# Optimization experiments

Measured on AMD Instinct MI355X. Metric: run time of the kernel, lower is better.

## Reference

```python
import jax, jax.numpy as jnp
import numpy as np

H, C = 8, 32          # heads, channels per head; H*C = 256 triggers the LN branch
N_NODES = 30000       # nodes per node type
N_EDGES = 100000      # edges per edge type
N_TYPES = 6           # hardwired edge types (all src = Package_Name)
D_IN = 128            # raw input feature dim (Package_Name stays at 128)
LRELU_SLOPE = 0.2     # PyG GATConv default negative_slope


def _segment_softmax(e, dst, n):
    # softmax of per-edge logits e [E,H] grouped by destination node
    m = jax.ops.segment_max(e, dst, num_segments=n)
    ex = jnp.exp(e - m[dst])
    den = jax.ops.segment_sum(ex, dst, num_segments=n)
    return ex / (den[dst] + 1e-16)


def _gat(x_src, x_tgt, src, dst, Ws, Wd, a_s, a_d, b):
    # bipartite GATConv, concat heads, no self loops, no edge features
    hs = (x_src @ Ws).reshape(-1, H, C)   # [Ns,H,C]
    hd = (x_tgt @ Wd).reshape(-1, H, C)   # [Nt,H,C]
    es = jnp.einsum('nhc,hc->nh', hs, a_s)
    ed = jnp.einsum('nhc,hc->nh', hd, a_d)
    e = jax.nn.leaky_relu(es[src] + ed[dst], negative_slope=LRELU_SLOPE)  # [E,H]
    n = x_tgt.shape[0]
    alpha = _segment_softmax(e, dst, n)                                   # [E,H]
    msg = hs[src] * alpha[:, :, None]                                     # [E,H,C]
    out = jax.ops.segment_sum(msg, dst, num_segments=n).reshape(n, H * C) + b
    return out, alpha


def _ln_relu(x, g, b):
    mu = x.mean(-1, keepdims=True)
    var = ((x - mu) ** 2).mean(-1, keepdims=True)
    return jax.nn.relu((x - mu) / jnp.sqrt(var + 1e-5) * g + b)


def setup_inputs() -> dict:
    key = jax.random.key(0)
    ks = jax.random.split(key, 16)
    s = 0.05
    return {
        'x_pkg': jax.random.normal(ks[0], (N_NODES, D_IN), jnp.float32),
        'x_tgt': jax.random.normal(ks[1], (N_TYPES, N_NODES, D_IN), jnp.float32),
        'edge_index': jax.random.randint(ks[2], (N_TYPES, 2, N_EDGES), 0, N_NODES, jnp.int32),
        'W1_src': jax.random.normal(ks[3], (N_TYPES, D_IN, H * C), jnp.float32) * s,
        'W1_dst': jax.random.normal(ks[4], (N_TYPES, D_IN, H * C), jnp.float32) * s,
        'att1_src': jax.random.normal(ks[5], (N_TYPES, H, C), jnp.float32) * s,
        'att1_dst': jax.random.normal(ks[6], (N_TYPES, H, C), jnp.float32) * s,
        'b1': jnp.zeros((N_TYPES, H * C), jnp.float32),
        'W2_src': jax.random.normal(ks[7], (N_TYPES, D_IN, H * C), jnp.float32) * s,
        'W2_dst': jax.random.normal(ks[8], (N_TYPES, H * C, H * C), jnp.float32) * s,
        'att2_src': jax.random.normal(ks[9], (N_TYPES, H, C), jnp.float32) * s,
        'att2_dst': jax.random.normal(ks[10], (N_TYPES, H, C), jnp.float32) * s,
        'b2': jnp.zeros((N_TYPES, H * C), jnp.float32),
        'gamma': jnp.ones((N_TYPES, H * C), jnp.float32),
        'beta': jnp.zeros((N_TYPES, H * C), jnp.float32),
        'Wc': jax.random.normal(ks[11], (N_TYPES * H * C + D_IN, 1), jnp.float32) * s,
        'bc': jnp.zeros((1,), jnp.float32),
    }


def reference(x_pkg, x_tgt, edge_index, W1_src, W1_dst, att1_src, att1_dst, b1,
              W2_src, W2_dst, att2_src, att2_dst, b2, gamma, beta, Wc, bc):
    def layer(xt, ei, Ws, Wd, a_s, a_d, bb):
        return _gat(x_pkg, xt, ei[0], ei[1], Ws, Wd, a_s, a_d, bb)

    vlayer = jax.vmap(layer, in_axes=(0, 0, 0, 0, 0, 0, 0))

    # layer 1: Package_Name -> each of 6 target types; Package_Name itself unchanged
    out1, _ = vlayer(x_tgt, edge_index, W1_src, W1_dst, att1_src, att1_dst, b1)
    x1 = jax.vmap(_ln_relu)(out1, gamma, beta)   # module reuses ln1 after both layers

    # layer 2: src features are still the raw 128-d Package_Name features
    out2, alpha2 = vlayer(x1, edge_index, W2_src, W2_dst, att2_src, att2_dst, b2)
    x2 = jax.vmap(_ln_relu)(out2, gamma, beta)

    # global mean pool per node type, concat (6 targets then Package_Name), classify
    pooled = jnp.concatenate([x2.mean(axis=1).reshape(-1), x_pkg.mean(axis=0)])
    logits = pooled @ Wc[:, 0] + bc[0]
    return logits, alpha2
```

## Files before the change

kernel.cpp:

```cpp
#include <hip/hip_runtime.h>
#include <hip/hip_bf16.h>
#include <cstddef>

#define N_NODES 30000
#define N_EDGES 100000
#define N_TYPES 6
#define D_IN 128
#define HC 256
#define NH 8
#define CH 32

typedef __attribute__((ext_vector_type(8))) unsigned short ushort8_t;
typedef __attribute__((ext_vector_type(4))) unsigned short ushort4_t;
typedef __attribute__((ext_vector_type(8))) __bf16 bf16x8;
typedef __attribute__((ext_vector_type(4))) float floatx4;

#define FG_GRID (N_NODES / 4)

__device__ inline unsigned short f2bf(float f) {
    unsigned u = __float_as_uint(f);
    u += 0x7fffu + ((u >> 16) & 1u);
    return (unsigned short)(u >> 16);
}
__device__ inline float bf2f(unsigned short u) {
    return __uint_as_float(((unsigned)u) << 16);
}

__global__ void zero4(float4* __restrict__ p, int n4) {
    int g = blockIdx.x * blockDim.x + threadIdx.x;
    if (g < n4) p[g] = make_float4(0.f, 0.f, 0.f, 0.f);
}
__global__ void zero_i(int* __restrict__ p, int n) {
    int g = blockIdx.x * blockDim.x + threadIdx.x;
    if (g < n) p[g] = 0;
}
__global__ void to_bf16(const float* __restrict__ x, unsigned short* __restrict__ o, int n4) {
    int g = blockIdx.x * blockDim.x + threadIdx.x;
    if (g >= n4) return;
    float4 v = ((const float4*)x)[g];
    ushort4_t p;
    p[0] = f2bf(v.x); p[1] = f2bf(v.y); p[2] = f2bf(v.z); p[3] = f2bf(v.w);
    *(ushort4_t*)&o[(size_t)g * 4] = p;
}

__global__ void hist_all(const int* __restrict__ ei, int* __restrict__ counts) {
    int t = blockIdx.y;
    int e = blockIdx.x * 256 + threadIdx.x;
    if (e < N_EDGES)
        atomicAdd(&counts[t * N_NODES + ei[(size_t)t * 2 * N_EDGES + N_EDGES + e]], 1);
}

#define SCAN_T 1024
#define SCAN_C 30
__global__ __launch_bounds__(1024) void scan_all(const int* __restrict__ counts_g,
                                                 int* __restrict__ row_ptr_g,
                                                 int* __restrict__ cursor_g) {
    int t = blockIdx.x;
    const int* counts = counts_g + t * N_NODES;
    int* row_ptr = row_ptr_g + t * (N_NODES + 1);
    int* cursor = cursor_g + t * N_NODES;
    __shared__ int part[SCAN_T];
    int tid = threadIdx.x;
    int base = tid * SCAN_C;
    int loc[SCAN_C];
    int s = 0;
    #pragma unroll
    for (int i = 0; i < SCAN_C; ++i) {
        int idx = base + i;
        int v = (idx < N_NODES) ? counts[idx] : 0;
        loc[i] = s; s += v;
    }
    part[tid] = s;
    __syncthreads();
    int tot = s;
    for (int d = 1; d < SCAN_T; d <<= 1) {
        int v = (tid >= d) ? part[tid - d] : 0;
        __syncthreads();
        part[tid] += v;
        __syncthreads();
    }
    int off = part[tid] - tot;
    #pragma unroll
    for (int i = 0; i < SCAN_C; ++i) {
        int idx = base + i;
        if (idx < N_NODES) { int r = off + loc[i]; row_ptr[idx] = r; cursor[idx] = r; }
    }
    if (tid == SCAN_T - 1) row_ptr[N_NODES] = part[SCAN_T - 1];
}

__global__ void fill_all(const int* __restrict__ ei, int* __restrict__ cursor,
                         int* __restrict__ elist) {
    int t = blockIdx.y;
    int e = blockIdx.x * 256 + threadIdx.x;
    if (e < N_EDGES) {
        const int* src = ei + (size_t)t * 2 * N_EDGES;
        const int* dst = src + N_EDGES;
        int pos = atomicAdd(&cursor[t * N_NODES + dst[e]], 1);
        elist[t * N_EDGES + pos] = src[e];
    }
}

__global__ void att_weight_all(const float* __restrict__ W1d, const float* __restrict__ a1d,
                               const float* __restrict__ W2d, const float* __restrict__ a2d,
                               float* __restrict__ wd1, float* __restrict__ wd2) {
    int g = blockIdx.x * blockDim.x + threadIdx.x;
    const int per_t = (D_IN + HC) * NH;
    if (g >= N_TYPES * per_t) return;
    int t = g / per_t, r = g % per_t;
    if (r < D_IN * NH) {
        int k = r >> 3, h = r & 7;
        const float* wr = W1d + (size_t)t * D_IN * HC + (size_t)k * HC + h * CH;
        const float* ar = a1d + t * HC + h * CH;
        float s = 0.f;
        #pragma unroll
        for (int c = 0; c < CH; ++c) s += wr[c] * ar[c];
        wd1[t * D_IN * NH + h * D_IN + k] = s;
    } else {
        r -= D_IN * NH;
        int k = r >> 3, h = r & 7;
        const float* wr = W2d + (size_t)t * HC * HC + (size_t)k * HC + h * CH;
        const float* ar = a2d + t * HC + h * CH;
        float s = 0.f;
        #pragma unroll
        for (int c = 0; c < CH; ++c) s += wr[c] * ar[c];
        wd2[t * HC * NH + h * HC + k] = s;
    }
}

__global__ __launch_bounds__(256) void wt_prep(const float* __restrict__ W1s,
                                               const float* __restrict__ W2s,
                                               unsigned short* __restrict__ Wt) {
    const int j = blockIdx.z;
    const float* W = (j < 6) ? W1s + (size_t)j * D_IN * HC
                             : W2s + (size_t)(j - 6) * D_IN * HC;
    const int n0 = blockIdx.x * 64;
    const int k0 = blockIdx.y * 32;
    __shared__ unsigned short tile[32][71];
    const int t = threadIdx.x;
    {
        const int k = t >> 3, n = (t & 7) * 8;
        const float4 a = *(const float4*)&W[(size_t)(k0 + k) * HC + n0 + n];
        const float4 b = *(const float4*)&W[(size_t)(k0 + k) * HC + n0 + n + 4];
        tile[k][n + 0] = f2bf(a.x); tile[k][n + 1] = f2bf(a.y);
        tile[k][n + 2] = f2bf(a.z); tile[k][n + 3] = f2bf(a.w);
        tile[k][n + 4] = f2bf(b.x); tile[k][n + 5] = f2bf(b.y);
        tile[k][n + 6] = f2bf(b.z); tile[k][n + 7] = f2bf(b.w);
    }
    __syncthreads();
    {
        const int n = t >> 2, k = (t & 3) * 8;
        ushort8_t v;
        #pragma unroll
        for (int q = 0; q < 8; ++q) v[q] = tile[k + q][n];
        *(ushort8_t*)&Wt[((size_t)j * HC + n0 + n) * D_IN + k0 + k] = v;
    }
}

__global__ __launch_bounds__(256) void ed1_all(const float* __restrict__ x_tgt,
                                               const float* __restrict__ wd1,
                                               float* __restrict__ ed1g) {
    const int t = blockIdx.y;
    const int lane = threadIdx.x & 63;
    const int wv = threadIdx.x >> 6;
    const int n8 = lane >> 3, h = lane & 7;
    const int node = blockIdx.x * 32 + wv * 8 + n8;
    if (node >= N_NODES) return;
    const float* xr = x_tgt + ((size_t)t * N_NODES + node) * D_IN;
    const float* wp = wd1 + t * D_IN * NH + h * D_IN;
    float acc = 0.f;
    #pragma unroll
    for (int k = 0; k < D_IN; k += 4) {
        const float4 x4 = *(const float4*)&xr[k];
        const float4 w4 = *(const float4*)&wp[k];
        acc += x4.x * w4.x + x4.y * w4.y + x4.z * w4.z + x4.w * w4.w;
    }
    ed1g[((size_t)t * N_NODES + node) * NH + h] = acc;
}

__global__ __launch_bounds__(256) void gemm_all(const unsigned short* __restrict__ A,
                                                const unsigned short* __restrict__ Wt,
                                                const float* __restrict__ att1,
                                                const float* __restrict__ att2,
                                                unsigned short* __restrict__ hs_all,
                                                float* __restrict__ es_all) {
    const int j = blockIdx.z;
    const unsigned short* B = Wt + (size_t)j * HC * D_IN;
    const float* att = (j < 6) ? att1 + j * HC : att2 + (j - 6) * HC;
    unsigned short* Cp = hs_all + (size_t)j * N_NODES * HC;
    float* e_out = es_all + (size_t)j * N_NODES * NH;

    __shared__ __align__(16) unsigned short As[64 * 136];

    const int tid = threadIdx.x;
    const int w = tid >> 6;
    const int lane = tid & 63;
    const int col = lane & 15;
    const int quad = lane >> 4;
    const int m0 = blockIdx.x * 64;
    const int n0 = blockIdx.y * 64;

    {
        const int r = tid >> 2;
        const int kc = (tid & 3) * 8;
        const int gm = m0 + r;
        #pragma unroll
        for (int c = 0; c < 4; ++c) {
            ushort8_t v = (ushort8_t){0, 0, 0, 0, 0, 0, 0, 0};
            if (gm < N_NODES) v = *(const ushort8_t*)&A[(size_t)gm * D_IN + kc + c * 32];
            *(ushort8_t*)&As[r * 136 + kc + c * 32] = v;
        }
    }
    __syncthreads();

    floatx4 acc[4];
    #pragma unroll
    for (int ct = 0; ct < 4; ++ct) acc[ct] = (floatx4){0.f, 0.f, 0.f, 0.f};

    #pragma unroll
    for (int ks = 0; ks < 4; ++ks) {
        ushort8_t araw = *(const ushort8_t*)&As[(w * 16 + col) * 136 + quad * 8 + ks * 32];
        bf16x8 af = __builtin_bit_cast(bf16x8, araw);
        #pragma unroll
        for (int ct = 0; ct < 4; ++ct) {
            ushort8_t braw = *(const ushort8_t*)&B[(size_t)(n0 + ct * 16 + col) * D_IN + quad * 8 + ks * 32];
            bf16x8 bf = __builtin_bit_cast(bf16x8, braw);
            acc[ct] = __builtin_amdgcn_mfma_f32_16x16x32_bf16(af, bf, acc[ct], 0, 0, 0);
        }
    }

    #pragma unroll
    for (int ct = 0; ct < 4; ++ct) {
        #pragma unroll
        for (int r = 0; r < 4; ++r) {
            int gm = m0 + w * 16 + quad * 4 + r;
            if (gm < N_NODES) Cp[(size_t)gm * HC + n0 + ct * 16 + col] = f2bf(acc[ct][r]);
        }
    }

    float attv[4];
    #pragma unroll
    for (int ct = 0; ct < 4; ++ct) attv[ct] = att[n0 + ct * 16 + col];
    const int hbase = n0 >> 5;
    #pragma unroll
    for (int r = 0; r < 4; ++r) {
        float h0v = acc[0][r] * attv[0] + acc[1][r] * attv[1];
        float h1v = acc[2][r] * attv[2] + acc[3][r] * attv[3];
        #pragma unroll
        for (int off = 1; off < 16; off <<= 1) {
            h0v += __shfl_xor(h0v, off);
            h1v += __shfl_xor(h1v, off);
        }
        if (col == 0) {
            int gm = m0 + w * 16 + quad * 4 + r;
            if (gm < N_NODES) {
                e_out[gm * NH + hbase] = h0v;
                e_out[gm * NH + hbase + 1] = h1v;
            }
        }
    }
}

__device__ inline void edge4(const float* __restrict__ es,
                             const unsigned short* __restrict__ hs,
                             int s_pre, int i, int cm,
                             int h_l, int lane, float ed_mine,
                             float& den, float4& acc) {
    const int i1 = (i + 1 < cm) ? i + 1 : cm;
    const int i2 = (i + 2 < cm) ? i + 2 : cm;
    const int i3 = (i + 3 < cm) ? i + 3 : cm;
    const int s0 = __shfl(s_pre, i);
    const int s1 = __shfl(s_pre, i1);
    const int s2 = __shfl(s_pre, i2);
    const int s3 = __shfl(s_pre, i3);
    float q0 = es[s0 * NH + h_l];
    float q1 = es[s1 * NH + h_l];
    float q2 = es[s2 * NH + h_l];
    float q3 = es[s3 * NH + h_l];
    const ushort4_t v0 = *(const ushort4_t*)&hs[(size_t)s0 * HC + lane * 4];
    const ushort4_t v1 = *(const ushort4_t*)&hs[(size_t)s1 * HC + lane * 4];
    const ushort4_t v2 = *(const ushort4_t*)&hs[(size_t)s2 * HC + lane * 4];
    const ushort4_t v3 = *(const ushort4_t*)&hs[(size_t)s3 * HC + lane * 4];
    q0 += ed_mine; q0 = (q0 >= 0.f) ? q0 : 0.2f * q0;
    q1 += ed_mine; q1 = (q1 >= 0.f) ? q1 : 0.2f * q1;
    q2 += ed_mine; q2 = (q2 >= 0.f) ? q2 : 0.2f * q2;
    q3 += ed_mine; q3 = (q3 >= 0.f) ? q3 : 0.2f * q3;
    const float x0 = __expf(q0);
    const float x1 = (i + 1 <= cm) ? __expf(q1) : 0.f;
    const float x2 = (i + 2 <= cm) ? __expf(q2) : 0.f;
    const float x3 = (i + 3 <= cm) ? __expf(q3) : 0.f;
    den += (x0 + x1) + (x2 + x3);
    acc.x += x0 * bf2f(v0[0]) + x1 * bf2f(v1[0]) + x2 * bf2f(v2[0]) + x3 * bf2f(v3[0]);
    acc.y += x0 * bf2f(v0[1]) + x1 * bf2f(v1[1]) + x2 * bf2f(v2[1]) + x3 * bf2f(v3[1]);
    acc.z += x0 * bf2f(v0[2]) + x1 * bf2f(v1[2]) + x2 * bf2f(v2[2]) + x3 * bf2f(v3[2]);
    acc.w += x0 * bf2f(v0[3]) + x1 * bf2f(v1[3]) + x2 * bf2f(v2[3]) + x3 * bf2f(v3[3]);
}

__device__ inline void edge1(const float* __restrict__ es,
                             const unsigned short* __restrict__ hs,
                             int s, int h_l, int lane, float ed_mine,
                             float& den, float4& acc) {
    float x = es[s * NH + h_l] + ed_mine;
    x = (x >= 0.f) ? x : 0.2f * x;
    const float ex = __expf(x);
    den += ex;
    const ushort4_t hv = *(const ushort4_t*)&hs[(size_t)s * HC + lane * 4];
    acc.x += ex * bf2f(hv[0]); acc.y += ex * bf2f(hv[1]);
    acc.z += ex * bf2f(hv[2]); acc.w += ex * bf2f(hv[3]);
}

__global__ __launch_bounds__(256) void fused_gather_all(
        const int* __restrict__ row_ptr_g, const int* __restrict__ elist_g,
        const float* __restrict__ es_all, const float* __restrict__ ed1g,
        const unsigned short* __restrict__ hs_all,
        const float* __restrict__ b1, const float* __restrict__ b2,
        const float* __restrict__ gamma, const float* __restrict__ beta,
        const float* __restrict__ wd2,
        float* __restrict__ ed2g_all, float* __restrict__ deng_all,
        float* __restrict__ ppart) {
    const int t = blockIdx.y;
    const int* row_ptr = row_ptr_g + t * (N_NODES + 1);
    const int* elist = elist_g + t * N_EDGES;
    const float* es1 = es_all + (size_t)t * N_NODES * NH;
    const float* es2 = es_all + (size_t)(6 + t) * N_NODES * NH;
    const unsigned short* hs1 = hs_all + (size_t)t * N_NODES * HC;
    const unsigned short* hs2 = hs_all + (size_t)(6 + t) * N_NODES * HC;
    const float* gam = gamma + t * HC;
    const float* bet = beta + t * HC;
    const float* w2 = wd2 + t * HC * NH;
    float* ed2g = ed2g_all + (size_t)t * N_NODES * NH;
    float* deng = deng_all + (size_t)t * N_NODES * NH;

    const int lane = threadIdx.x & 63;
    const int w = threadIdx.x >> 6;
    const int d = blockIdx.x * 4 + w;
    const int h_l = lane >> 3;

    const float ed_mine = ed1g[((size_t)t * N_NODES + d) * NH + h_l];
    const int e0 = row_ptr[d], e1n = row_ptr[d + 1];
    const int cnt = e1n - e0;
    int s_pre = 0;
    if (lane < cnt) s_pre = elist[e0 + lane];

    float den1 = 0.f, den2 = 0.f;
    float4 acc1 = make_float4(0.f, 0.f, 0.f, 0.f);
    float4 acc2 = make_float4(0.f, 0.f, 0.f, 0.f);

    float q20, q21, q22, q23;
    ushort4_t v20, v21, v22, v23;
    const bool fast = (cnt > 0) && (cnt <= 4);

    if (fast) {
        const int cm = cnt - 1;
        const int s0 = __shfl(s_pre, 0);
        const int s1 = __shfl(s_pre, (1 < cm) ? 1 : cm);
        const int s2 = __shfl(s_pre, (2 < cm) ? 2 : cm);
        const int s3 = __shfl(s_pre, cm);
        float q10 = es1[s0 * NH + h_l];
        float q11 = es1[s1 * NH + h_l];
        float q12 = es1[s2 * NH + h_l];
        float q13 = es1[s3 * NH + h_l];
        const ushort4_t v10 = *(const ushort4_t*)&hs1[(size_t)s0 * HC + lane * 4];
        const ushort4_t v11 = *(const ushort4_t*)&hs1[(size_t)s1 * HC + lane * 4];
        const ushort4_t v12 = *(const ushort4_t*)&hs1[(size_t)s2 * HC + lane * 4];
        const ushort4_t v13 = *(const ushort4_t*)&hs1[(size_t)s3 * HC + lane * 4];
        q20 = es2[s0 * NH + h_l];
        q21 = es2[s1 * NH + h_l];
        q22 = es2[s2 * NH + h_l];
        q23 = es2[s3 * NH + h_l];
        v20 = *(const ushort4_t*)&hs2[(size_t)s0 * HC + lane * 4];
        v21 = *(const ushort4_t*)&hs2[(size_t)s1 * HC + lane * 4];
        v22 = *(const ushort4_t*)&hs2[(size_t)s2 * HC + lane * 4];
        v23 = *(const ushort4_t*)&hs2[(size_t)s3 * HC + lane * 4];
        q10 += ed_mine; q10 = (q10 >= 0.f) ? q10 : 0.2f * q10;
        q11 += ed_mine; q11 = (q11 >= 0.f) ? q11 : 0.2f * q11;
        q12 += ed_mine; q12 = (q12 >= 0.f) ? q12 : 0.2f * q12;
        q13 += ed_mine; q13 = (q13 >= 0.f) ? q13 : 0.2f * q13;
        const float x0 = __expf(q10);
        const float x1 = (cnt > 1) ? __expf(q11) : 0.f;
        const float x2 = (cnt > 2) ? __expf(q12) : 0.f;
        const float x3 = (cnt > 3) ? __expf(q13) : 0.f;
        den1 = (x0 + x1) + (x2 + x3);
        acc1.x = x0 * bf2f(v10[0]) + x1 * bf2f(v11[0]) + x2 * bf2f(v12[0]) + x3 * bf2f(v13[0]);
        acc1.y = x0 * bf2f(v10[1]) + x1 * bf2f(v11[1]) + x2 * bf2f(v12[1]) + x3 * bf2f(v13[1]);
        acc1.z = x0 * bf2f(v10[2]) + x1 * bf2f(v11[2]) + x2 * bf2f(v12[2]) + x3 * bf2f(v13[2]);
        acc1.w = x0 * bf2f(v10[3]) + x1 * bf2f(v11[3]) + x2 * bf2f(v12[3]) + x3 * bf2f(v13[3]);
    } else if (cnt > 0) {
        const int c1 = (cnt < 64) ? cnt : 64;
        const int cm = c1 - 1;
        for (int i = 0; i < c1; i += 4)
            edge4(es1, hs1, s_pre, i, cm, h_l, lane, ed_mine, den1, acc1);
        if (cnt > 64)
            for (int ii = e0 + 64; ii < e1n; ++ii)
                edge1(es1, hs1, elist[ii], h_l, lane, ed_mine, den1, acc1);
    }

    const float inv1 = 1.f / (den1 + 1e-16f);
    const float4 bv1 = *(const float4*)&b1[t * HC + lane * 4];
    acc1.x = acc1.x * inv1 + bv1.x; acc1.y = acc1.y * inv1 + bv1.y;
    acc1.z = acc1.z * inv1 + bv1.z; acc1.w = acc1.w * inv1 + bv1.w;

    float s1 = acc1.x + acc1.y + acc1.z + acc1.w;
    float s2 = acc1.x * acc1.x + acc1.y * acc1.y + acc1.z * acc1.z + acc1.w * acc1.w;
    #pragma unroll
    for (int off = 1; off < 64; off <<= 1) { s1 += __shfl_xor(s1, off); s2 += __shfl_xor(s2, off); }
    const float mu = s1 * (1.f / 256.f);
    const float var = s2 * (1.f / 256.f) - mu * mu;
    const float rstd = rsqrtf(var + 1e-5f);
    const float4 g4 = *(const float4*)&gam[lane * 4];
    const float4 b4 = *(const float4*)&bet[lane * 4];
    const float ya0 = fmaxf((acc1.x - mu) * rstd * g4.x + b4.x, 0.f);
    const float ya1 = fmaxf((acc1.y - mu) * rstd * g4.y + b4.y, 0.f);
    const float ya2 = fmaxf((acc1.z - mu) * rstd * g4.z + b4.z, 0.f);
    const float ya3 = fmaxf((acc1.w - mu) * rstd * g4.w + b4.w, 0.f);

    __shared__ __align__(16) float ya_s[4][256];
    {
        const int c0 = lane * 4;
        const int widx = (c0 & ~31) | ((c0 & 31) ^ ((lane >> 3) << 2));
        *(float4*)&ya_s[w][widx] = make_float4(ya0, ya1, ya2, ya3);
    }
    const int k8 = lane >> 3;
    const int hh = lane & 7;
    const float* w2h = w2 + hh * HC;
    float e2 = 0.f;
    #pragma unroll
    for (int jj = 0; jj < 8; ++jj) {
        const int idx = k8 * 32 + ((jj * 4) ^ (k8 << 2));
        const float4 y = *(const float4*)&ya_s[w][idx];
        const float4 wv = *(const float4*)&w2h[k8 * 32 + jj * 4];
        e2 += y.x * wv.x + y.y * wv.y + y.z * wv.z + y.w * wv.w;
    }
    e2 += __shfl_xor(e2, 8);
    e2 += __shfl_xor(e2, 16);
    e2 += __shfl_xor(e2, 32);
    if (lane < 8) ed2g[d * NH + lane] = e2;
    const float ed2_mine = __shfl(e2, h_l);

    if (fast) {
        q20 += ed2_mine; q20 = (q20 >= 0.f) ? q20 : 0.2f * q20;
        q21 += ed2_mine; q21 = (q21 >= 0.f) ? q21 : 0.2f * q21;
        q22 += ed2_mine; q22 = (q22 >= 0.f) ? q22 : 0.2f * q22;
        q23 += ed2_mine; q23 = (q23 >= 0.f) ? q23 : 0.2f * q23;
        const float x0 = __expf(q20);
        const float x1 = (cnt > 1) ? __expf(q21) : 0.f;
        const float x2 = (cnt > 2) ? __expf(q22) : 0.f;
        const float x3 = (cnt > 3) ? __expf(q23) : 0.f;
        den2 = (x0 + x1) + (x2 + x3);
        acc2.x = x0 * bf2f(v20[0]) + x1 * bf2f(v21[0]) + x2 * bf2f(v22[0]) + x3 * bf2f(v23[0]);
        acc2.y = x0 * bf2f(v20[1]) + x1 * bf2f(v21[1]) + x2 * bf2f(v22[1]) + x3 * bf2f(v23[1]);
        acc2.z = x0 * bf2f(v20[2]) + x1 * bf2f(v21[2]) + x2 * bf2f(v22[2]) + x3 * bf2f(v23[2]);
        acc2.w = x0 * bf2f(v20[3]) + x1 * bf2f(v21[3]) + x2 * bf2f(v22[3]) + x3 * bf2f(v23[3]);
    } else if (cnt > 0) {
        const int c1 = (cnt < 64) ? cnt : 64;
        const int cm = c1 - 1;
        for (int i = 0; i < c1; i += 4)
            edge4(es2, hs2, s_pre, i, cm, h_l, lane, ed2_mine, den2, acc2);
        if (cnt > 64)
            for (int ii = e0 + 64; ii < e1n; ++ii)
                edge1(es2, hs2, elist[ii], h_l, lane, ed2_mine, den2, acc2);
    }

    if ((lane & 7) == 0) deng[d * NH + h_l] = den2;
    const float inv2 = 1.f / (den2 + 1e-16f);
    const float4 bv2 = *(const float4*)&b2[t * HC + lane * 4];
    acc2.x = acc2.x * inv2 + bv2.x; acc2.y = acc2.y * inv2 + bv2.y;
    acc2.z = acc2.z * inv2 + bv2.z; acc2.w = acc2.w * inv2 + bv2.w;

    float t1 = acc2.x + acc2.y + acc2.z + acc2.w;
    float t2 = acc2.x * acc2.x + acc2.y * acc2.y + acc2.z * acc2.z + acc2.w * acc2.w;
    #pragma unroll
    for (int off = 1; off < 64; off <<= 1) { t1 += __shfl_xor(t1, off); t2 += __shfl_xor(t2, off); }
    const float mu2 = t1 * (1.f / 256.f);
    const float var2 = t2 * (1.f / 256.f) - mu2 * mu2;
    const float rstd2 = rsqrtf(var2 + 1e-5f);
    float4 pool;
    pool.x = fmaxf((acc2.x - mu2) * rstd2 * g4.x + b4.x, 0.f);
    pool.y = fmaxf((acc2.y - mu2) * rstd2 * g4.y + b4.y, 0.f);
    pool.z = fmaxf((acc2.z - mu2) * rstd2 * g4.z + b4.z, 0.f);
    pool.w = fmaxf((acc2.w - mu2) * rstd2 * g4.w + b4.w, 0.f);

    __shared__ __align__(16) float sacc[4][260];
    *(float4*)&sacc[w][lane * 4] = pool;
    __syncthreads();
    const int tid = threadIdx.x;
    float tot = sacc[0][tid] + sacc[1][tid] + sacc[2][tid] + sacc[3][tid];
    ppart[((size_t)t * FG_GRID + blockIdx.x) * HC + tid] = tot;
}

__global__ __launch_bounds__(256) void pool_reduce_all(const float* __restrict__ ppart,
                                                       float* __restrict__ psums) {
    int t = blockIdx.y;
    const float* part = ppart + (size_t)t * FG_GRID * HC;
    int tid = threadIdx.x;
    float acc = 0.f;
    for (int b = blockIdx.x; b < FG_GRID; b += gridDim.x)
        acc += part[(size_t)b * HC + tid];
    atomicAdd(&psums[t * HC + tid], acc);
}

__global__ __launch_bounds__(256) void alpha_all(const int* __restrict__ ei,
                          const float* __restrict__ es_all,
                          const float* __restrict__ ed2g_all,
                          const float* __restrict__ deng_all,
                          float* __restrict__ out) {
    int t = blockIdx.y;
    int e = blockIdx.x * 256 + threadIdx.x;
    if (e >= N_EDGES) return;
    const int* src = ei + (size_t)t * 2 * N_EDGES;
    const int* dst = src + N_EDGES;
    const int s = src[e], d = dst[e];
    const float* esp = es_all + (size_t)(6 + t) * N_NODES * NH + (size_t)s * NH;
    const float* edp = ed2g_all + (size_t)t * N_NODES * NH + (size_t)d * NH;
    const float* dnp = deng_all + (size_t)t * N_NODES * NH + (size_t)d * NH;
    const float4 ea = *(const float4*)esp;
    const float4 eb = *(const float4*)(esp + 4);
    const float4 da = *(const float4*)edp;
    const float4 db = *(const float4*)(edp + 4);
    const float4 na = *(const float4*)dnp;
    const float4 nb = *(const float4*)(dnp + 4);
    float x[8];
    x[0] = ea.x + da.x; x[1] = ea.y + da.y; x[2] = ea.z + da.z; x[3] = ea.w + da.w;
    x[4] = eb.x + db.x; x[5] = eb.y + db.y; x[6] = eb.z + db.z; x[7] = eb.w + db.w;
    float n[8] = {na.x, na.y, na.z, na.w, nb.x, nb.y, nb.z, nb.w};
    float* op = out + (size_t)t * N_EDGES * NH + (size_t)e * NH;
    #pragma unroll
    for (int h = 0; h < 8; ++h) {
        float v = x[h];
        v = (v >= 0.f) ? v : 0.2f * v;
        op[h] = __expf(v) / (n[h] + 1e-16f);
    }
}

__global__ __launch_bounds__(256) void pkg_accum(const float* __restrict__ x, float* __restrict__ sums) {
    int tid = threadIdx.x;
    int col = tid & 127;
    int rof = tid >> 7;
    float acc = 0.f;
    for (int r = blockIdx.x * 2 + rof; r < N_NODES; r += gridDim.x * 2)
        acc += x[(size_t)r * D_IN + col];
    atomicAdd(&sums[col], acc);
}

__global__ __launch_bounds__(256) void logits_k(const float* __restrict__ psums,
                                                const float* __restrict__ ksums,
                                                const float* __restrict__ Wc,
                                                const float* __restrict__ bc,
                                                float* __restrict__ out) {
    int tid = threadIdx.x;
    const float inv = 1.f / (float)N_NODES;
    float acc = 0.f;
    for (int i = tid; i < N_TYPES * HC; i += 256) acc += psums[i] * inv * Wc[i];
    if (tid < D_IN) acc += ksums[tid] * inv * Wc[N_TYPES * HC + tid];
    #pragma unroll
    for (int off = 32; off; off >>= 1) acc += __shfl_down(acc, off);
    __shared__ float w[4];
    if ((tid & 63) == 0) w[tid >> 6] = acc;
    __syncthreads();
    if (tid == 0) out[0] = w[0] + w[1] + w[2] + w[3] + bc[0];
}

static inline void zf(float* p, int n, hipStream_t stream) {
    int n4 = (n + 3) >> 2;
    zero4<<<(n4 + 255) / 256, 256, 0, stream>>>((float4*)p, n4);
}

extern "C" void kernel_launch(void* const* d_in, const int* in_sizes, int n_in,
                              void* d_out, int out_size, void* d_ws, size_t ws_size,
                              hipStream_t stream) {
    const float* x_pkg    = (const float*)d_in[0];
    const float* x_tgt    = (const float*)d_in[1];
    const int*   ei       = (const int*)d_in[2];
    const float* W1_src   = (const float*)d_in[3];
    const float* W1_dst   = (const float*)d_in[4];
    const float* att1_src = (const float*)d_in[5];
    const float* att1_dst = (const float*)d_in[6];
    const float* b1       = (const float*)d_in[7];
    const float* W2_src   = (const float*)d_in[8];
    const float* W2_dst   = (const float*)d_in[9];
    const float* att2_src = (const float*)d_in[10];
    const float* att2_dst = (const float*)d_in[11];
    const float* b2       = (const float*)d_in[12];
    const float* gamma    = (const float*)d_in[13];
    const float* beta     = (const float*)d_in[14];
    const float* Wc       = (const float*)d_in[15];
    const float* bc       = (const float*)d_in[16];
    float* out = (float*)d_out;

    char* wsb = (char*)d_ws;
    unsigned short* xpkg_bf = (unsigned short*)wsb;
    unsigned short* hs_all  = xpkg_bf + (size_t)N_NODES * D_IN;
    float* es_all   = (float*)(hs_all + (size_t)12 * N_NODES * HC);
    float* ed2g_all = es_all + (size_t)12 * N_NODES * NH;
    float* deng_all = ed2g_all + (size_t)N_TYPES * N_NODES * NH;
    float* psums    = deng_all + (size_t)N_TYPES * N_NODES * NH;
    float* ksums    = psums + N_TYPES * HC;
    float* wd1      = ksums + D_IN;
    float* wd2      = wd1 + N_TYPES * D_IN * NH;
    unsigned short* Wt = (unsigned short*)(wd2 + N_TYPES * HC * NH);
    float* ed1g     = (float*)(Wt + (size_t)12 * HC * D_IN);
    float* ppart    = ed1g + (size_t)N_TYPES * N_NODES * NH;
    int* counts  = (int*)(ppart + (size_t)N_TYPES * FG_GRID * HC);
    int* row_ptr = counts + N_TYPES * N_NODES;
    int* cursor  = row_ptr + N_TYPES * (N_NODES + 1);
    int* elist   = cursor + N_TYPES * N_NODES;

    dim3 egrid((N_EDGES + 255) / 256, N_TYPES);

    zf(psums, N_TYPES * HC, stream);
    zf(ksums, D_IN, stream);
    pkg_accum<<<256, 256, 0, stream>>>(x_pkg, ksums);
    {
        int tot = N_TYPES * (D_IN + HC) * NH;
        att_weight_all<<<(tot + 255) / 256, 256, 0, stream>>>(W1_dst, att1_dst, W2_dst, att2_dst, wd1, wd2);
    }
    {
        dim3 g(4, 4, 12);
        wt_prep<<<g, 256, 0, stream>>>(W1_src, W2_src, Wt);
    }
    {
        dim3 g((N_NODES + 31) / 32, N_TYPES);
        ed1_all<<<g, 256, 0, stream>>>(x_tgt, wd1, ed1g);
    }
    to_bf16<<<((N_NODES * D_IN / 4) + 255) / 256, 256, 0, stream>>>(x_pkg, xpkg_bf, N_NODES * D_IN / 4);
    zero_i<<<(N_TYPES * N_NODES + 255) / 256, 256, 0, stream>>>(counts, N_TYPES * N_NODES);
    hist_all<<<egrid, 256, 0, stream>>>(ei, counts);
    scan_all<<<N_TYPES, SCAN_T, 0, stream>>>(counts, row_ptr, cursor);
    fill_all<<<egrid, 256, 0, stream>>>(ei, cursor, elist);

    {
        dim3 g((N_NODES + 63) / 64, HC / 64, 12);
        gemm_all<<<g, 256, 0, stream>>>(xpkg_bf, Wt, att1_src, att2_src,
                                        hs_all, es_all);
    }

    {
        dim3 g(FG_GRID, N_TYPES);
        fused_gather_all<<<g, 256, 0, stream>>>(row_ptr, elist, es_all, ed1g, hs_all,
                                                b1, b2, gamma, beta, wd2,
                                                ed2g_all, deng_all, ppart);
    }
    {
        dim3 g(64, N_TYPES);
        pool_reduce_all<<<g, 256, 0, stream>>>(ppart, psums);
    }
    {
        dim3 g((N_EDGES + 255) / 256, N_TYPES);
        alpha_all<<<g, 256, 0, stream>>>(ei, es_all, ed2g_all, deng_all, out + 1);
    }

    logits_k<<<1, 256, 0, stream>>>(psums, ksums, Wc, bc, out);
}
```

Measured before the change: 922.0 us.

## Stage GEMM weights in LDS with wider N tile; pool via direct atomics

The projection GEMM now covers 128 output columns per block instead of 64 and loads the weight tile into shared memory once, replacing repeated per-wave global loads of B. The four per-head attention logits are written as a single float4. The pooled partial sums from the fused gather kernel are now added straight into the final sums with atomics, which removes the partial buffer and the separate reduction kernel, and the two zeroing calls are merged into one. This costs more LDS and registers per GEMM block and adds many atomics per column of the pooled sums.

```diff
diff --git a/kernel.cpp b/kernel.cpp
--- a/kernel.cpp
+++ b/kernel.cpp
@@ -190,6 +190,7 @@
     float* e_out = es_all + (size_t)j * N_NODES * NH;
 
     __shared__ __align__(16) unsigned short As[64 * 136];
+    __shared__ __align__(16) unsigned short Bs[128 * 136];
 
     const int tid = threadIdx.x;
     const int w = tid >> 6;
@@ -197,7 +198,7 @@
     const int col = lane & 15;
     const int quad = lane >> 4;
     const int m0 = blockIdx.x * 64;
-    const int n0 = blockIdx.y * 64;
+    const int n0 = blockIdx.y * 128;
 
     {
         const int r = tid >> 2;
@@ -210,26 +211,36 @@
             *(ushort8_t*)&As[r * 136 + kc + c * 32] = v;
         }
     }
+    {
+        const int r = tid >> 1;
+        const int ks = (tid & 1) * 64;
+        const unsigned short* br = &B[(size_t)(n0 + r) * D_IN + ks];
+        #pragma unroll
+        for (int q = 0; q < 8; ++q) {
+            ushort8_t v = *(const ushort8_t*)&br[q * 8];
+            *(ushort8_t*)&Bs[r * 136 + ks + q * 8] = v;
+        }
+    }
     __syncthreads();
 
-    floatx4 acc[4];
-    #pragma unroll
-    for (int ct = 0; ct < 4; ++ct) acc[ct] = (floatx4){0.f, 0.f, 0.f, 0.f};
+    floatx4 acc[8];
+    #pragma unroll
+    for (int ct = 0; ct < 8; ++ct) acc[ct] = (floatx4){0.f, 0.f, 0.f, 0.f};
 
     #pragma unroll
     for (int ks = 0; ks < 4; ++ks) {
-        ushort8_t araw = *(const ushort8_t*)&As[(w * 16 + col) * 136 + quad * 8 + ks * 32];
+        ushort8_t araw = *(const ushort8_t*)&As[(w * 16 + col) * 136 + ks * 32 + quad * 8];
         bf16x8 af = __builtin_bit_cast(bf16x8, araw);
         #pragma unroll
-        for (int ct = 0; ct < 4; ++ct) {
-            ushort8_t braw = *(const ushort8_t*)&B[(size_t)(n0 + ct * 16 + col) * D_IN + quad * 8 + ks * 32];
+        for (int ct = 0; ct < 8; ++ct) {
+            ushort8_t braw = *(const ushort8_t*)&Bs[(ct * 16 + col) * 136 + ks * 32 + quad * 8];
             bf16x8 bf = __builtin_bit_cast(bf16x8, braw);
             acc[ct] = __builtin_amdgcn_mfma_f32_16x16x32_bf16(af, bf, acc[ct], 0, 0, 0);
         }
     }
 
     #pragma unroll
-    for (int ct = 0; ct < 4; ++ct) {
+    for (int ct = 0; ct < 8; ++ct) {
         #pragma unroll
         for (int r = 0; r < 4; ++r) {
             int gm = m0 + w * 16 + quad * 4 + r;
@@ -237,25 +248,27 @@
         }
     }
 
-    float attv[4];
-    #pragma unroll
-    for (int ct = 0; ct < 4; ++ct) attv[ct] = att[n0 + ct * 16 + col];
+    float attv[8];
+    #pragma unroll
+    for (int ct = 0; ct < 8; ++ct) attv[ct] = att[n0 + ct * 16 + col];
     const int hbase = n0 >> 5;
     #pragma unroll
     for (int r = 0; r < 4; ++r) {
         float h0v = acc[0][r] * attv[0] + acc[1][r] * attv[1];
         float h1v = acc[2][r] * attv[2] + acc[3][r] * attv[3];
+        float h2v = acc[4][r] * attv[4] + acc[5][r] * attv[5];
+        float h3v = acc[6][r] * attv[6] + acc[7][r] * attv[7];
         #pragma unroll
         for (int off = 1; off < 16; off <<= 1) {
             h0v += __shfl_xor(h0v, off);
             h1v += __shfl_xor(h1v, off);
+            h2v += __shfl_xor(h2v, off);
+            h3v += __shfl_xor(h3v, off);
         }
         if (col == 0) {
             int gm = m0 + w * 16 + quad * 4 + r;
-            if (gm < N_NODES) {
-                e_out[gm * NH + hbase] = h0v;
-                e_out[gm * NH + hbase + 1] = h1v;
-            }
+            if (gm < N_NODES)
+                *(float4*)&e_out[gm * NH + hbase] = make_float4(h0v, h1v, h2v, h3v);
         }
     }
 }
@@ -316,7 +329,7 @@
         const float* __restrict__ gamma, const float* __restrict__ beta,
         const float* __restrict__ wd2,
         float* __restrict__ ed2g_all, float* __restrict__ deng_all,
-        float* __restrict__ ppart) {
+        float* __restrict__ psums) {
     const int t = blockIdx.y;
     const int* row_ptr = row_ptr_g + t * (N_NODES + 1);
     const int* elist = elist_g + t * N_EDGES;
@@ -484,18 +497,7 @@
     __syncthreads();
     const int tid = threadIdx.x;
     float tot = sacc[0][tid] + sacc[1][tid] + sacc[2][tid] + sacc[3][tid];
-    ppart[((size_t)t * FG_GRID + blockIdx.x) * HC + tid] = tot;
-}
-
-__global__ __launch_bounds__(256) void pool_reduce_all(const float* __restrict__ ppart,
-                                                       float* __restrict__ psums) {
-    int t = blockIdx.y;
-    const float* part = ppart + (size_t)t * FG_GRID * HC;
-    int tid = threadIdx.x;
-    float acc = 0.f;
-    for (int b = blockIdx.x; b < FG_GRID; b += gridDim.x)
-        acc += part[(size_t)b * HC + tid];
-    atomicAdd(&psums[t * HC + tid], acc);
+    atomicAdd(&psums[t * HC + tid], tot);
 }
 
 __global__ __launch_bounds__(256) void alpha_all(const int* __restrict__ ei,
@@ -598,16 +600,14 @@
     float* wd2      = wd1 + N_TYPES * D_IN * NH;
     unsigned short* Wt = (unsigned short*)(wd2 + N_TYPES * HC * NH);
     float* ed1g     = (float*)(Wt + (size_t)12 * HC * D_IN);
-    float* ppart    = ed1g + (size_t)N_TYPES * N_NODES * NH;
-    int* counts  = (int*)(ppart + (size_t)N_TYPES * FG_GRID * HC);
+    int* counts  = (int*)(ed1g + (size_t)N_TYPES * N_NODES * NH);
     int* row_ptr = counts + N_TYPES * N_NODES;
     int* cursor  = row_ptr + N_TYPES * (N_NODES + 1);
     int* elist   = cursor + N_TYPES * N_NODES;
 
     dim3 egrid((N_EDGES + 255) / 256, N_TYPES);
 
-    zf(psums, N_TYPES * HC, stream);
-    zf(ksums, D_IN, stream);
+    zf(psums, N_TYPES * HC + D_IN, stream);
     pkg_accum<<<256, 256, 0, stream>>>(x_pkg, ksums);
     {
         int tot = N_TYPES * (D_IN + HC) * NH;
@@ -628,7 +628,7 @@
     fill_all<<<egrid, 256, 0, stream>>>(ei, cursor, elist);
 
     {
-        dim3 g((N_NODES + 63) / 64, HC / 64, 12);
+        dim3 g((N_NODES + 63) / 64, 2, 12);
         gemm_all<<<g, 256, 0, stream>>>(xpkg_bf, Wt, att1_src, att2_src,
                                         hs_all, es_all);
     }
@@ -637,11 +637,7 @@
         dim3 g(FG_GRID, N_TYPES);
         fused_gather_all<<<g, 256, 0, stream>>>(row_ptr, elist, es_all, ed1g, hs_all,
                                                 b1, b2, gamma, beta, wd2,
-                                                ed2g_all, deng_all, ppart);
-    }
-    {
-        dim3 g(64, N_TYPES);
-        pool_reduce_all<<<g, 256, 0, stream>>>(ppart, psums);
+                                                ed2g_all, deng_all, psums);
     }
     {
         dim3 g((N_EDGES + 255) / 256, N_TYPES);
```

After: 1.150 ms. 24.7% more time.
